# Optimization experiments

Measured on AMD Instinct MI355X. Metric: run time of the kernel, lower is better.

Reference implementation:

```python
import jax, jax.numpy as jnp
import numpy as np

BIT = 128
Y_P = 0.5
RIGHT = BIT / 8.0
LEFT = RIGHT / 2.0
UB = BIT / 2.0
ALPHA = 0.1
PCT_NUM, PCT_DEN = 9, 10  # percent = 9/10
C_COEF = (1.0 / RIGHT) * np.log(Y_P / (99.0 * (1.0 - Y_P)))  # slope c (constant since y_p fixed)
A_COEF = -1.0 / (LEFT * C_COEF) * np.log(99.0 * Y_P / (1.0 - Y_P))  # hard-branch factor a
# with y_p=0.5: d = -c*BP, g = -a*c*BP, so f_easy = c*(x-BP), f_hard = a*c*(x-BP)


def setup_inputs() -> dict:
    key = jax.random.key(0)
    k1, k2 = jax.random.split(key)
    N, C = 6144, 200
    u = jax.random.normal(k1, (N, BIT), dtype=jnp.float32)
    labels = jax.random.randint(k2, (N,), 0, C)
    y = jax.nn.one_hot(labels, C, dtype=jnp.int32)
    ind = jnp.arange(N, dtype=jnp.int32)  # unused dataset indices
    return {"u": u, "y": y, "ind": ind}


def reference(u, y, ind):
    sg = jax.lax.stop_gradient
    N = u.shape[0]
    uh = jnp.tanh(u)
    s = (y @ y.T) > 0                      # [N,N] bool similarity (diagonal is True)
    inner = uh @ uh.T                      # [N,N]
    n_sim = s.sum(axis=1)                  # int per-row similar count
    n_dis = N - n_sim
    fn_sim = n_sim.astype(jnp.float32)
    fn_dis = n_dis.astype(jnp.float32)
    idx = jnp.arange(N)[None, :]

    meanS = jnp.clip(jnp.where(s, inner, 0.0).sum(1) / jnp.maximum(fn_sim, 1.0), 0.0, UB)
    meanDS = jnp.clip(jnp.where(s, 0.0, inner).sum(1) / jnp.maximum(fn_dis, 1.0), 0.0, UB)

    dis_sorted = jnp.sort(jnp.where(s, -jnp.inf, inner), axis=1)
    start_dis = (n_dis * PCT_NUM) // PCT_DEN          # int(len*0.9)
    tail_mask = idx >= (N - n_dis + start_dis)[:, None]
    tail_cnt = jnp.maximum((n_dis - start_dis).astype(jnp.float32), 1.0)
    dMax = jnp.clip(jnp.where(tail_mask, dis_sorted, 0.0).sum(1) / tail_cnt, 0.0, UB)

    sim_sorted = jnp.sort(jnp.where(s, inner, jnp.inf), axis=1)
    start_sim = (n_sim * PCT_NUM) // PCT_DEN
    head_mask = idx < (n_sim - start_sim)[:, None]
    head_cnt = jnp.maximum((n_sim - start_sim).astype(jnp.float32), 1.0)
    sMin = jnp.clip(jnp.where(head_mask, sim_sorted, 0.0).sum(1) / head_cnt, 0.0, UB)

    # .item() in the original detaches these -> stop_gradient
    meanS, meanDS, dMax, sMin = map(sg, (meanS, meanDS, dMax, sMin))
    BP = meanS - (UB - meanS) / UB * jnp.abs(meanS - dMax)      # [N]
    BPd = meanDS + meanDS / UB * jnp.abs(meanDS - sMin)         # [N]

    # similar-pair loss: f + log(1+exp(-f)) == softplus(f)
    dc = inner - BP[:, None]
    f_sim = jnp.where(inner > BP[:, None], C_COEF * dc, A_COEF * C_COEF * dc)
    mask_sim = s & (inner != BP[:, None])             # == BP excluded in torch indexing
    cnt_sim = jnp.maximum(mask_sim.sum(1).astype(jnp.float32), 1.0)
    row_pos = jnp.where(mask_sim, jax.nn.softplus(f_sim), 0.0).sum(1) / cnt_sim

    # dissimilar-pair loss: log(1+exp(-f)) == softplus(-f)
    dcd = inner - BPd[:, None]
    f_dis = jnp.where(inner < BPd[:, None], C_COEF * dcd, A_COEF * C_COEF * dcd)
    mask_dis = (~s) & (inner != BPd[:, None])
    cnt_dis = jnp.maximum(mask_dis.sum(1).astype(jnp.float32), 1.0)
    row_neg = jnp.where(mask_dis, jax.nn.softplus(-f_dis), 0.0).sum(1) / cnt_dis

    valid = (n_sim > 0) & (n_dis > 0)
    count = valid.sum().astype(jnp.float32)
    posL = jnp.where(count > 0, jnp.where(valid, row_pos, 0.0).sum() / jnp.maximum(count, 1.0), 0.0)
    navL = jnp.where(count > 0, jnp.where(valid, row_neg, 0.0).sum() / jnp.maximum(count, 1.0), 0.0)

    q_loss = ALPHA * jnp.mean((uh - jnp.sign(uh)) ** 2)
    return posL + navL + q_loss
```

## Files before the change

### kernel.cpp

```cpp
#include <hip/hip_runtime.h>
#include <cstdint>

#define NROW 6144
#define KDIM 128
#define NLAB 200
#define C_COEF (-0.28719499063341177f)
#define UBV 64.0f

typedef _Float16 f16x8 __attribute__((ext_vector_type(8)));
typedef _Float16 f16x2 __attribute__((ext_vector_type(2)));
typedef float f32x4 __attribute__((ext_vector_type(4)));
typedef __attribute__((address_space(1))) const void as1c_void;
typedef __attribute__((address_space(3))) void as3_void;

union U8 { f16x8 h; unsigned u[4]; f16x2 p[4]; };
union CV16 { _Float16 h; unsigned short us; };

__device__ __forceinline__ float softplus_f(float x){
  return fmaxf(x, 0.f) + __logf(1.f + __expf(-fabsf(x)));
}
__device__ __forceinline__ float waveRedF(float v){
#pragma unroll
  for (int o = 32; o; o >>= 1) v += __shfl_down(v, o, 64);
  return v;
}
__device__ __forceinline__ float bfRedF(float v){
#pragma unroll
  for (int o = 32; o; o >>= 1) v += __shfl_xor(v, o, 64);
  return v;
}
__device__ __forceinline__ int bfRedI(int v){
#pragma unroll
  for (int o = 32; o; o >>= 1) v += __shfl_xor(v, o, 64);
  return v;
}
__device__ __forceinline__ int bfMaxI(int v){
#pragma unroll
  for (int o = 32; o; o >>= 1){ int x = __shfl_xor(v, o, 64); v = v > x ? v : x; }
  return v;
}
__device__ __forceinline__ float bfMaxF(float v){
#pragma unroll
  for (int o = 32; o; o >>= 1) v = fmaxf(v, __shfl_xor(v, o, 64));
  return v;
}
__device__ __forceinline__ float val_of_key(unsigned key){
  unsigned bits = (key & 0x8000u) ? (key ^ 0x8000u) : (key ^ 0xFFFFu);
  CV16 cv; cv.us = (unsigned short)bits;
  return (float)cv.h;
}

__global__ __launch_bounds__(256) void k_labtanh(const int* __restrict__ y,
    unsigned char* __restrict__ lab, int* __restrict__ cnt, int* __restrict__ simIdx,
    const float* __restrict__ u, _Float16* __restrict__ uhswz, float* __restrict__ accf){
  const int bid = blockIdx.x;
  const int tid = threadIdx.x;
  if (bid < NROW){
    if (tid < NLAB && y[(size_t)bid * NLAB + tid] != 0){
      lab[bid] = (unsigned char)tid;
      int p = atomicAdd(&cnt[tid], 1);
      if (p < 512) simIdx[tid * 512 + p] = bid;
    }
    return;
  }
  const int gid = (bid - NROW) * 256 + tid;
  const int row = gid >> 4;
  const int h = gid & 15;
  const int g = h ^ (row & 7);
  const float* sp = u + (size_t)row * KDIM + g * 8;
  float q = 0.f;
  f16x8 o;
#pragma unroll
  for (int t = 0; t < 8; t++){
    float x = sp[t];
    float e2 = __expf(2.f * x);
    float th = 1.f - 2.f * __builtin_amdgcn_rcpf(e2 + 1.f);
    float sg = (th > 0.f) ? 1.f : ((th < 0.f) ? -1.f : 0.f);
    float d = th - sg;
    q += d * d;
    o[t] = (_Float16)th;
  }
  *(f16x8*)(uhswz + (size_t)row * KDIM + h * 8) = o;
  q = waveRedF(q);
  __shared__ float qb[4];
  if ((tid & 63) == 0) qb[tid >> 6] = q;
  __syncthreads();
  if (tid == 0) atomicAdd(&accf[0], qb[0] + qb[1] + qb[2] + qb[3]);
}

__global__ __launch_bounds__(256) void k_mm(const _Float16* __restrict__ A,
    _Float16* __restrict__ out, int row0){
  __shared__ __align__(16) _Float16 SH[2 * 128 * KDIM];
  _Float16* As = SH;
  _Float16* Bs = SH + 128 * KDIM;
  const int tid = threadIdx.x;
  const int wav = tid >> 6, lane = tid & 63;
  const int bj = blockIdx.x, bi = blockIdx.y;

  const char* Ag = (const char*)(A + (size_t)(row0 + bi * 128) * KDIM);
  const char* Bg = (const char*)(A + (size_t)(bj * 128) * KDIM);
  char* Asb = (char*)As;
  char* Bsb = (char*)Bs;
#pragma unroll
  for (int t = 0; t < 8; t++){
    const int ub = wav * 8192 + t * 1024;
    __builtin_amdgcn_global_load_lds((as1c_void*)(Ag + ub + lane * 16),
                                     (as3_void*)(Asb + ub), 16, 0, 0);
    __builtin_amdgcn_global_load_lds((as1c_void*)(Bg + ub + lane * 16),
                                     (as3_void*)(Bsb + ub), 16, 0, 0);
  }
  __syncthreads();

  const int quad = lane >> 4, l16 = lane & 15;
  const int wm = (wav >> 1) * 64, wn = (wav & 1) * 64;
  f32x4 acc[4][4];
#pragma unroll
  for (int im = 0; im < 4; im++)
#pragma unroll
    for (int in = 0; in < 4; in++)
      acc[im][in] = (f32x4){0.f, 0.f, 0.f, 0.f};

#pragma unroll
  for (int kb = 0; kb < 4; kb++){
    f16x8 af[4], bf[4];
#pragma unroll
    for (int i = 0; i < 4; i++){
      const int m = wm + i * 16 + l16;
      const int gidx = kb * 4 + quad;
      af[i] = *(const f16x8*)(Asb + m * 256 + ((gidx ^ (m & 7)) << 4));
      const int n = wn + i * 16 + l16;
      bf[i] = *(const f16x8*)(Bsb + n * 256 + ((gidx ^ (n & 7)) << 4));
    }
#pragma unroll
    for (int im = 0; im < 4; im++)
#pragma unroll
      for (int in = 0; in < 4; in++)
        acc[im][in] = __builtin_amdgcn_mfma_f32_16x16x32_f16(af[im], bf[in], acc[im][in], 0, 0, 0);
  }
  __syncthreads();

  _Float16* Cs = SH;
#pragma unroll
  for (int im = 0; im < 4; im++)
#pragma unroll
    for (int in = 0; in < 4; in++)
#pragma unroll
      for (int r = 0; r < 4; r++){
        const int rl = wm + im * 16 + quad * 4 + r;
        const int cl = wn + in * 16 + l16;
        Cs[rl * 132 + cl] = (_Float16)acc[im][in][r];
      }
  __syncthreads();

  _Float16* obase = out + (size_t)(bi * 128) * NROW + (size_t)bj * 128;
  const int s = tid & 15;
#pragma unroll
  for (int i = 0; i < 8; i++){
    const int r = (tid >> 4) + i * 16;
    f16x8 vv = *(const f16x8*)(Cs + r * 132 + s * 8);
    *(f16x8*)(obase + (size_t)r * NROW + s * 8) = vv;
  }
}

__global__ __launch_bounds__(256) void k_stats(const _Float16* __restrict__ buf,
    const unsigned char* __restrict__ lab, const int* __restrict__ cnt,
    const int* __restrict__ simIdx, float* __restrict__ rowRes, int row0){
  __shared__ int   histS[4][1028];
  __shared__ float simvS[4][512];
  const int tid = threadIdx.x;
  const int lane = tid & 63;
  const int wav = tid >> 6;
  const int lrow = blockIdx.x * 4 + wav;
  const int row = row0 + lrow;
  const int myl = lab[row];
  const int n_sim = cnt[myl];
  const int n_dis = NROW - n_sim;
  if (n_dis == 0 || n_sim == 0) return;
  const int k1 = n_dis - (n_dis * 9) / 10;
  const int k2 = n_sim - (n_sim * 9) / 10;
  const int ns = (n_sim < 512) ? n_sim : 512;

  int*   hist = histS[wav];
  int*   myh  = hist + (lane >> 4) * 257;
  float* simv = simvS[wav];
#pragma unroll
  for (int r = 0; r < 4; r++) *(int4*)&hist[(lane + 64 * r) * 4] = make_int4(0, 0, 0, 0);
  if (lane == 0) *(int4*)&hist[1024] = make_int4(0, 0, 0, 0);

  const f16x8* src = (const f16x8*)(buf + (size_t)lrow * NROW);
  const _Float16* srcs = buf + (size_t)lrow * NROW;

  float sumAll = 0.f;
  const f16x2 ones = (f16x2){(_Float16)1.f, (_Float16)1.f};
#pragma unroll 1
  for (int it = 0; it < 12; ++it){
    U8 x; x.h = src[it * 64 + lane];
#pragma unroll
    for (int k = 0; k < 4; k++){
      unsigned wv = x.u[k];
      unsigned m = (wv >> 15) & 0x00010001u;
      unsigned key2 = wv ^ 0x80008000u ^ (m * 0x7FFFu);
      atomicAdd(&myh[(key2 >> 8) & 0xFFu], 1);
      atomicAdd(&myh[key2 >> 24], 1);
#if __has_builtin(__builtin_amdgcn_fdot2)
      sumAll = __builtin_amdgcn_fdot2(x.p[k], ones, sumAll, false);
#else
      sumAll += (float)x.h[2 * k] + (float)x.h[2 * k + 1];
#endif
    }
  }

  float sumS = 0.f;
  for (int t = lane; t < ns; t += 64){
    int idx = simIdx[myl * 512 + t];
    CV16 cv; cv.h = srcs[idx];
    unsigned bits = (unsigned)cv.us;
    unsigned key = bits ^ 0x8000u ^ ((bits >> 15) * 0x7FFFu);
    float v = (float)cv.h;
    simv[t] = v; sumS += v;
    atomicAdd(&myh[key >> 8], -1);
  }
  sumAll = bfRedF(sumAll);
  sumS = bfRedF(sumS);
  const float sumD = sumAll - sumS;

  int cArr[4];
#pragma unroll
  for (int d = 0; d < 4; d++){
    const int b = 4 * lane + d;
    cArr[d] = hist[b] + hist[257 + b] + hist[514 + b] + hist[771 + b];
  }
  int part = cArr[0] + cArr[1] + cArr[2] + cArr[3];
  int suf = part;
#pragma unroll
  for (int o = 1; o < 64; o <<= 1){
    int x = __shfl_down(suf, o, 64);
    if (lane + o < 64) suf += x;
  }
  int cum = suf - part;
  int encB = -1, krF = 0;
#pragma unroll
  for (int d = 3; d >= 0; --d){
    int cd = cArr[d];
    if (k1 > cum && k1 <= cum + cd){ encB = 4 * lane + d; krF = k1 - cum; }
    cum += cd;
  }
  const int hbStar = bfMaxI(encB);
  const int kr1 = bfMaxI(krF);

#pragma unroll
  for (int r = 0; r < 4; r++) *(int4*)&hist[(lane + 64 * r) * 4] = make_int4(0, 0, 0, 0);
  if (lane == 0) *(int4*)&hist[1024] = make_int4(0, 0, 0, 0);

  float sAb = 0.f;
#pragma unroll 1
  for (int it = 0; it < 12; ++it){
    U8 x; x.h = src[it * 64 + lane];
#pragma unroll
    for (int k = 0; k < 4; k++){
      unsigned wv = x.u[k];
      unsigned m = (wv >> 15) & 0x00010001u;
      unsigned key2 = wv ^ 0x80008000u ^ (m * 0x7FFFu);
      int hbLo = (key2 >> 8) & 0xFF;
      int hbHi = key2 >> 24;
      if (hbLo > hbStar) sAb += (float)x.h[2 * k];
      else if (hbLo == hbStar) atomicAdd(&myh[key2 & 0xFFu], 1);
      if (hbHi > hbStar) sAb += (float)x.h[2 * k + 1];
      else if (hbHi == hbStar) atomicAdd(&myh[(key2 >> 16) & 0xFFu], 1);
    }
  }
  for (int t = lane; t < ns; t += 64){
    float v = simv[t];
    CV16 cv; cv.h = (_Float16)v;
    unsigned bits = (unsigned)cv.us;
    unsigned key = bits ^ 0x8000u ^ ((bits >> 15) * 0x7FFFu);
    int hb = (int)(key >> 8);
    if (hb > hbStar) sAb -= v;
    else if (hb == hbStar) atomicAdd(&myh[key & 0xFFu], -1);
  }
  sAb = bfRedF(sAb);

  int c2[4];
#pragma unroll
  for (int d = 0; d < 4; d++){
    const int b = 4 * lane + d;
    c2[d] = hist[b] + hist[257 + b] + hist[514 + b] + hist[771 + b];
  }
  part = c2[0] + c2[1] + c2[2] + c2[3];
  suf = part;
#pragma unroll
  for (int o = 1; o < 64; o <<= 1){
    int x = __shfl_down(suf, o, 64);
    if (lane + o < 64) suf += x;
  }
  cum = suf - part;
  int encL = -1, g2F = 0;
#pragma unroll
  for (int d = 3; d >= 0; --d){
    int cd = c2[d];
    if (kr1 > cum && kr1 <= cum + cd){ encL = 4 * lane + d; g2F = cum; }
    cum += cd;
  }
  const int lbStar = bfMaxI(encL);
  const int gt2 = bfMaxI(g2F);
  float sumIn = 0.f;
#pragma unroll
  for (int d = 0; d < 4; d++){
    int lb = 4 * lane + d;
    if (lb > lbStar) sumIn += (float)c2[d] * val_of_key((unsigned)((hbStar << 8) | lb));
  }
  sumIn = bfRedF(sumIn);
  const float piv = val_of_key((unsigned)((hbStar << 8) | lbStar));
  const float dSum = sAb + sumIn + (float)(kr1 - gt2) * piv;

  float fpiv2 = -3e38f; int flt = 0;
  for (int t = lane; t < ns; t += 64){
    float vt = simv[t];
    int lt = 0, eq = 0;
    for (int j = 0; j < ns; j++){
      float vj = simv[j];
      lt += (vj < vt); eq += (vj == vt);
    }
    if (lt < k2 && k2 <= lt + eq){ fpiv2 = vt; flt = lt; }
  }
  const float piv2 = bfMaxF(fpiv2);
  const int ltS = bfMaxI(flt);
  float slt = 0.f;
  for (int t = lane; t < ns; t += 64){
    float v = simv[t];
    if (v < piv2) slt += v;
  }
  slt = bfRedF(slt);
  const float sSum = slt + (float)(k2 - ltS) * piv2;

  const float meanS  = fminf(fmaxf(sumS / fmaxf((float)n_sim, 1.f), 0.f), UBV);
  const float meanDS = fminf(fmaxf(sumD / fmaxf((float)n_dis, 1.f), 0.f), UBV);
  const float dMax   = fminf(fmaxf(dSum / fmaxf((float)k1, 1.f), 0.f), UBV);
  const float sMin   = fminf(fmaxf(sSum / fmaxf((float)k2, 1.f), 0.f), UBV);
  const float BP  = meanS - (UBV - meanS) / UBV * fabsf(meanS - dMax);
  const float BPd = meanDS + meanDS / UBV * fabsf(meanDS - sMin);

  float an = 0.f; int ties = 0;
#pragma unroll 1
  for (int it = 0; it < 12; ++it){
    f16x8 h8 = src[it * 64 + lane];
#pragma unroll
    for (int e = 0; e < 8; e++){
      float v = (float)h8[e];
      float dcd = v - BPd;
      float f = ((dcd < 0.f) ? C_COEF : 2.f * C_COEF) * dcd;
      an += softplus_f(-f);
      ties += (dcd == 0.f);
    }
  }
  float spSim = 0.f; int tiesSim = 0;
  float ap = 0.f, cp = 0.f;
  for (int t = lane; t < ns; t += 64){
    float v = simv[t];
    float dcd = v - BPd;
    if (dcd == 0.f) tiesSim++;
    else {
      float f = ((dcd < 0.f) ? C_COEF : 2.f * C_COEF) * dcd;
      spSim += softplus_f(-f);
    }
    if (v != BP){
      float dc = v - BP;
      float f = (v > BP) ? C_COEF * dc : (2.f * C_COEF) * dc;
      ap += softplus_f(f); cp += 1.f;
    }
  }
  an = bfRedF(an); spSim = bfRedF(spSim);
  const int tiesT = bfRedI(ties);
  const int tiesSimT = bfRedI(tiesSim);
  ap = bfRedF(ap); cp = bfRedF(cp);
  if (lane == 0){
    const float L = __logf(1.f + __expf(-0.f));
    float anF = an - (float)tiesT * L - spSim;
    float cnF = (float)(n_dis - (tiesT - tiesSimT));
    float4 r;
    r.x = ap / fmaxf(cp, 1.f);
    r.y = anF / fmaxf(cnF, 1.f);
    r.z = 1.f;
    r.w = 0.f;
    *(float4*)(rowRes + 4 * (size_t)row) = r;
  }
}

__global__ __launch_bounds__(256) void k_final(const float* __restrict__ accf,
    const float* __restrict__ rowRes, float* __restrict__ out){
  const int tid = threadIdx.x;
  float p = 0.f, n = 0.f, c = 0.f;
  for (int i = tid; i < NROW; i += 256){
    float4 r = *(const float4*)(rowRes + 4 * (size_t)i);
    p += r.x; n += r.y; c += r.z;
  }
  p = bfRedF(p); n = bfRedF(n); c = bfRedF(c);
  __shared__ float sb[12];
  const int wav = tid >> 6;
  if ((tid & 63) == 0){ sb[wav] = p; sb[4 + wav] = n; sb[8 + wav] = c; }
  __syncthreads();
  if (tid == 0){
    p = sb[0] + sb[1] + sb[2] + sb[3];
    n = sb[4] + sb[5] + sb[6] + sb[7];
    c = sb[8] + sb[9] + sb[10] + sb[11];
    float posL = 0.f, navL = 0.f;
    if (c > 0.f){ posL = p / c; navL = n / c; }
    out[0] = posL + navL + 0.1f * (accf[0] / (float)(NROW * KDIM));
  }
}

extern "C" void kernel_launch(void* const* d_in, const int* in_sizes, int n_in,
                              void* d_out, int out_size, void* d_ws, size_t ws_size,
                              hipStream_t stream){
  const float* u = (const float*)d_in[0];
  const int* y = (const int*)d_in[1];
  char* ws = (char*)d_ws;
  float* accf = (float*)ws;
  int* cnt = (int*)(ws + 64);
  float* rowRes = (float*)(ws + 4096);
  unsigned char* lab = (unsigned char*)(ws + 102400);
  int* simIdx = (int*)(ws + 108544);
  _Float16* uhswz = (_Float16*)(ws + 518144);
  const size_t ibufOff = 518144 + (size_t)NROW * KDIM * 2;
  _Float16* ibuf = (_Float16*)(ws + ibufOff);

  hipMemsetAsync(d_ws, 0, 102400, stream);
  k_labtanh<<<NROW + (NROW * 16) / 256, 256, 0, stream>>>(y, lab, cnt, simIdx,
                                                          u, uhswz, accf);

  size_t avail = (ws_size > ibufOff) ? ws_size - ibufOff : 0;
  long maxRows = (long)(avail / ((size_t)NROW * 2));
  maxRows = (maxRows / 128) * 128;
  if (maxRows > NROW) maxRows = NROW;
  if (maxRows < 128) maxRows = 128;

  for (int r0 = 0; r0 < NROW; r0 += (int)maxRows){
    int rows = NROW - r0;
    if (rows > maxRows) rows = (int)maxRows;
    k_mm<<<dim3(48, rows / 128), 256, 0, stream>>>(uhswz, ibuf, r0);
    k_stats<<<rows / 4, 256, 0, stream>>>(ibuf, lab, cnt, simIdx, rowRes, r0);
  }
  k_final<<<1, 256, 0, stream>>>(accf, rowRes, (float*)d_out);
}
```

Measured before the change: 170.8 us.

## Process one row per block in stats kernel with row cached in LDS

The stats kernel now assigns a whole 256-thread block to each row instead of one wavefront per row. The row is staged once into shared memory so the second and third passes, and the similar-index gather, read LDS instead of global memory. Reductions now go through cross-wave shared buffers with block barriers, and the second-level histogram is shared by the block. The label kernel is also changed to handle four rows per block using int4 loads. The risk is lower per-block parallelism per row being offset by barrier overhead and higher LDS use per block, which could reduce occupancy.

```diff
diff --git a/kernel.cpp b/kernel.cpp
--- a/kernel.cpp
+++ b/kernel.cpp
@@ -29,19 +29,9 @@
   for (int o = 32; o; o >>= 1) v += __shfl_xor(v, o, 64);
   return v;
 }
-__device__ __forceinline__ int bfRedI(int v){
-#pragma unroll
-  for (int o = 32; o; o >>= 1) v += __shfl_xor(v, o, 64);
-  return v;
-}
 __device__ __forceinline__ int bfMaxI(int v){
 #pragma unroll
   for (int o = 32; o; o >>= 1){ int x = __shfl_xor(v, o, 64); v = v > x ? v : x; }
-  return v;
-}
-__device__ __forceinline__ float bfMaxF(float v){
-#pragma unroll
-  for (int o = 32; o; o >>= 1) v = fmaxf(v, __shfl_xor(v, o, 64));
   return v;
 }
 __device__ __forceinline__ float val_of_key(unsigned key){
@@ -55,15 +45,26 @@
     const float* __restrict__ u, _Float16* __restrict__ uhswz, float* __restrict__ accf){
   const int bid = blockIdx.x;
   const int tid = threadIdx.x;
-  if (bid < NROW){
-    if (tid < NLAB && y[(size_t)bid * NLAB + tid] != 0){
-      lab[bid] = (unsigned char)tid;
-      int p = atomicAdd(&cnt[tid], 1);
-      if (p < 512) simIdx[tid * 512 + p] = bid;
+  const int NLB = NROW / 4;
+  if (bid < NLB){
+    const int lane = tid & 63;
+    const int row = bid * 4 + (tid >> 6);
+    if (lane < NLAB / 4){
+      const int4 v = ((const int4*)(y + (size_t)row * NLAB))[lane];
+      int t = -1;
+      if (v.x != 0) t = 4 * lane;
+      if (v.y != 0) t = 4 * lane + 1;
+      if (v.z != 0) t = 4 * lane + 2;
+      if (v.w != 0) t = 4 * lane + 3;
+      if (t >= 0){
+        lab[row] = (unsigned char)t;
+        int p = atomicAdd(&cnt[t], 1);
+        if (p < 512) simIdx[t * 512 + p] = row;
+      }
     }
     return;
   }
-  const int gid = (bid - NROW) * 256 + tid;
+  const int gid = (bid - NLB) * 256 + tid;
   const int row = gid >> 4;
   const int h = gid & 15;
   const int g = h ^ (row & 7);
@@ -165,12 +166,17 @@
 __global__ __launch_bounds__(256) void k_stats(const _Float16* __restrict__ buf,
     const unsigned char* __restrict__ lab, const int* __restrict__ cnt,
     const int* __restrict__ simIdx, float* __restrict__ rowRes, int row0){
-  __shared__ int   histS[4][1028];
-  __shared__ float simvS[4][512];
+  __shared__ __align__(16) _Float16 rowh[NROW];
+  __shared__ int   hist[4][257];
+  __shared__ int   hist2[257];
+  __shared__ float simv[512];
+  __shared__ float rbuf[32];
+  __shared__ float ctlF[2];
+  __shared__ int   ctlI[2];
   const int tid = threadIdx.x;
   const int lane = tid & 63;
   const int wav = tid >> 6;
-  const int lrow = blockIdx.x * 4 + wav;
+  const int lrow = blockIdx.x;
   const int row = row0 + lrow;
   const int myl = lab[row];
   const int n_sim = cnt[myl];
@@ -180,21 +186,22 @@
   const int k2 = n_sim - (n_sim * 9) / 10;
   const int ns = (n_sim < 512) ? n_sim : 512;
 
-  int*   hist = histS[wav];
-  int*   myh  = hist + (lane >> 4) * 257;
-  float* simv = simvS[wav];
-#pragma unroll
-  for (int r = 0; r < 4; r++) *(int4*)&hist[(lane + 64 * r) * 4] = make_int4(0, 0, 0, 0);
-  if (lane == 0) *(int4*)&hist[1024] = make_int4(0, 0, 0, 0);
+  int* myh = hist[wav];
+#pragma unroll
+  for (int r = 0; r < 4; r++) myh[lane + 64 * r] = 0;
+  if (lane == 0) myh[256] = 0;
+  if (tid < 256) hist2[tid] = 0;
+  if (tid == 0) hist2[256] = 0;
+  __syncthreads();
 
   const f16x8* src = (const f16x8*)(buf + (size_t)lrow * NROW);
-  const _Float16* srcs = buf + (size_t)lrow * NROW;
-
   float sumAll = 0.f;
   const f16x2 ones = (f16x2){(_Float16)1.f, (_Float16)1.f};
-#pragma unroll 1
-  for (int it = 0; it < 12; ++it){
-    U8 x; x.h = src[it * 64 + lane];
+#pragma unroll
+  for (int it = 0; it < 3; ++it){
+    const int g8 = it * 256 + tid;
+    U8 x; x.h = src[g8];
+    ((f16x8*)rowh)[g8] = x.h;
 #pragma unroll
     for (int k = 0; k < 4; k++){
       unsigned wv = x.u[k];
@@ -209,26 +216,38 @@
 #endif
     }
   }
+  sumAll = waveRedF(sumAll);
+  if (lane == 0) rbuf[wav] = sumAll;
+  __syncthreads();
 
   float sumS = 0.f;
-  for (int t = lane; t < ns; t += 64){
+  for (int t = tid; t < ns; t += 256){
     int idx = simIdx[myl * 512 + t];
-    CV16 cv; cv.h = srcs[idx];
+    CV16 cv; cv.h = rowh[idx];
     unsigned bits = (unsigned)cv.us;
     unsigned key = bits ^ 0x8000u ^ ((bits >> 15) * 0x7FFFu);
     float v = (float)cv.h;
     simv[t] = v; sumS += v;
     atomicAdd(&myh[key >> 8], -1);
   }
-  sumAll = bfRedF(sumAll);
-  sumS = bfRedF(sumS);
-  const float sumD = sumAll - sumS;
+  sumS = waveRedF(sumS);
+  if (lane == 0) rbuf[4 + wav] = sumS;
+  __syncthreads();
+
+  const float sumAllT = rbuf[0] + rbuf[1] + rbuf[2] + rbuf[3];
+  const float sumST   = rbuf[4] + rbuf[5] + rbuf[6] + rbuf[7];
+  const float sumD = sumAllT - sumST;
 
   int cArr[4];
-#pragma unroll
-  for (int d = 0; d < 4; d++){
-    const int b = 4 * lane + d;
-    cArr[d] = hist[b] + hist[257 + b] + hist[514 + b] + hist[771 + b];
+  {
+    int4 a = *(const int4*)&hist[0][4 * lane];
+    int4 b = *(const int4*)&hist[1][4 * lane];
+    int4 c = *(const int4*)&hist[2][4 * lane];
+    int4 d = *(const int4*)&hist[3][4 * lane];
+    cArr[0] = a.x + b.x + c.x + d.x;
+    cArr[1] = a.y + b.y + c.y + d.y;
+    cArr[2] = a.z + b.z + c.z + d.z;
+    cArr[3] = a.w + b.w + c.w + d.w;
   }
   int part = cArr[0] + cArr[1] + cArr[2] + cArr[3];
   int suf = part;
@@ -248,14 +267,10 @@
   const int hbStar = bfMaxI(encB);
   const int kr1 = bfMaxI(krF);
 
-#pragma unroll
-  for (int r = 0; r < 4; r++) *(int4*)&hist[(lane + 64 * r) * 4] = make_int4(0, 0, 0, 0);
-  if (lane == 0) *(int4*)&hist[1024] = make_int4(0, 0, 0, 0);
-
   float sAb = 0.f;
-#pragma unroll 1
-  for (int it = 0; it < 12; ++it){
-    U8 x; x.h = src[it * 64 + lane];
+#pragma unroll
+  for (int it = 0; it < 3; ++it){
+    U8 x; x.h = ((const f16x8*)rowh)[it * 256 + tid];
 #pragma unroll
     for (int k = 0; k < 4; k++){
       unsigned wv = x.u[k];
@@ -264,28 +279,28 @@
       int hbLo = (key2 >> 8) & 0xFF;
       int hbHi = key2 >> 24;
       if (hbLo > hbStar) sAb += (float)x.h[2 * k];
-      else if (hbLo == hbStar) atomicAdd(&myh[key2 & 0xFFu], 1);
+      else if (hbLo == hbStar) atomicAdd(&hist2[key2 & 0xFFu], 1);
       if (hbHi > hbStar) sAb += (float)x.h[2 * k + 1];
-      else if (hbHi == hbStar) atomicAdd(&myh[(key2 >> 16) & 0xFFu], 1);
-    }
-  }
-  for (int t = lane; t < ns; t += 64){
+      else if (hbHi == hbStar) atomicAdd(&hist2[(key2 >> 16) & 0xFFu], 1);
+    }
+  }
+  for (int t = tid; t < ns; t += 256){
     float v = simv[t];
     CV16 cv; cv.h = (_Float16)v;
     unsigned bits = (unsigned)cv.us;
     unsigned key = bits ^ 0x8000u ^ ((bits >> 15) * 0x7FFFu);
     int hb = (int)(key >> 8);
     if (hb > hbStar) sAb -= v;
-    else if (hb == hbStar) atomicAdd(&myh[key & 0xFFu], -1);
-  }
-  sAb = bfRedF(sAb);
+    else if (hb == hbStar) atomicAdd(&hist2[key & 0xFFu], -1);
+  }
+  sAb = waveRedF(sAb);
+  if (lane == 0) rbuf[8 + wav] = sAb;
+  __syncthreads();
+  const float sAbT = rbuf[8] + rbuf[9] + rbuf[10] + rbuf[11];
 
   int c2[4];
-#pragma unroll
-  for (int d = 0; d < 4; d++){
-    const int b = 4 * lane + d;
-    c2[d] = hist[b] + hist[257 + b] + hist[514 + b] + hist[771 + b];
-  }
+  { int4 c4 = *(const int4*)&hist2[4 * lane];
+    c2[0] = c4.x; c2[1] = c4.y; c2[2] = c4.z; c2[3] = c4.w; }
   part = c2[0] + c2[1] + c2[2] + c2[3];
   suf = part;
 #pragma unroll
@@ -311,29 +326,32 @@
   }
   sumIn = bfRedF(sumIn);
   const float piv = val_of_key((unsigned)((hbStar << 8) | lbStar));
-  const float dSum = sAb + sumIn + (float)(kr1 - gt2) * piv;
-
-  float fpiv2 = -3e38f; int flt = 0;
-  for (int t = lane; t < ns; t += 64){
+  const float dSum = sAbT + sumIn + (float)(kr1 - gt2) * piv;
+
+  for (int t = tid; t < ns; t += 256){
     float vt = simv[t];
     int lt = 0, eq = 0;
     for (int j = 0; j < ns; j++){
       float vj = simv[j];
       lt += (vj < vt); eq += (vj == vt);
     }
-    if (lt < k2 && k2 <= lt + eq){ fpiv2 = vt; flt = lt; }
-  }
-  const float piv2 = bfMaxF(fpiv2);
-  const int ltS = bfMaxI(flt);
+    if (lt < k2 && k2 <= lt + eq){ ctlF[0] = vt; ctlI[0] = lt; }
+  }
+  __syncthreads();
+  const float piv2 = ctlF[0];
+  const int ltS = ctlI[0];
   float slt = 0.f;
-  for (int t = lane; t < ns; t += 64){
+  for (int t = tid; t < ns; t += 256){
     float v = simv[t];
     if (v < piv2) slt += v;
   }
-  slt = bfRedF(slt);
-  const float sSum = slt + (float)(k2 - ltS) * piv2;
-
-  const float meanS  = fminf(fmaxf(sumS / fmaxf((float)n_sim, 1.f), 0.f), UBV);
+  slt = waveRedF(slt);
+  if (lane == 0) rbuf[12 + wav] = slt;
+  __syncthreads();
+  const float sltT = rbuf[12] + rbuf[13] + rbuf[14] + rbuf[15];
+  const float sSum = sltT + (float)(k2 - ltS) * piv2;
+
+  const float meanS  = fminf(fmaxf(sumST / fmaxf((float)n_sim, 1.f), 0.f), UBV);
   const float meanDS = fminf(fmaxf(sumD / fmaxf((float)n_dis, 1.f), 0.f), UBV);
   const float dMax   = fminf(fmaxf(dSum / fmaxf((float)k1, 1.f), 0.f), UBV);
   const float sMin   = fminf(fmaxf(sSum / fmaxf((float)k2, 1.f), 0.f), UBV);
@@ -341,9 +359,9 @@
   const float BPd = meanDS + meanDS / UBV * fabsf(meanDS - sMin);
 
   float an = 0.f; int ties = 0;
-#pragma unroll 1
-  for (int it = 0; it < 12; ++it){
-    f16x8 h8 = src[it * 64 + lane];
+#pragma unroll
+  for (int it = 0; it < 3; ++it){
+    f16x8 h8 = ((const f16x8*)rowh)[it * 256 + tid];
 #pragma unroll
     for (int e = 0; e < 8; e++){
       float v = (float)h8[e];
@@ -355,7 +373,7 @@
   }
   float spSim = 0.f; int tiesSim = 0;
   float ap = 0.f, cp = 0.f;
-  for (int t = lane; t < ns; t += 64){
+  for (int t = tid; t < ns; t += 256){
     float v = simv[t];
     float dcd = v - BPd;
     if (dcd == 0.f) tiesSim++;
@@ -369,16 +387,27 @@
       ap += softplus_f(f); cp += 1.f;
     }
   }
-  an = bfRedF(an); spSim = bfRedF(spSim);
-  const int tiesT = bfRedI(ties);
-  const int tiesSimT = bfRedI(tiesSim);
-  ap = bfRedF(ap); cp = bfRedF(cp);
+  an = waveRedF(an); ap = waveRedF(ap); cp = waveRedF(cp);
+  spSim = waveRedF(spSim);
+  float tiesF = waveRedF((float)ties);
+  float tiesSimF = waveRedF((float)tiesSim);
   if (lane == 0){
+    rbuf[wav] = an; rbuf[4 + wav] = ap; rbuf[8 + wav] = cp;
+    rbuf[16 + wav] = spSim; rbuf[20 + wav] = tiesF; rbuf[24 + wav] = tiesSimF;
+  }
+  __syncthreads();
+  if (tid == 0){
+    float anT = rbuf[0] + rbuf[1] + rbuf[2] + rbuf[3];
+    float apT = rbuf[4] + rbuf[5] + rbuf[6] + rbuf[7];
+    float cpT = rbuf[8] + rbuf[9] + rbuf[10] + rbuf[11];
+    float spT = rbuf[16] + rbuf[17] + rbuf[18] + rbuf[19];
+    float tiesT = rbuf[20] + rbuf[21] + rbuf[22] + rbuf[23];
+    float tiesSimT = rbuf[24] + rbuf[25] + rbuf[26] + rbuf[27];
     const float L = __logf(1.f + __expf(-0.f));
-    float anF = an - (float)tiesT * L - spSim;
-    float cnF = (float)(n_dis - (tiesT - tiesSimT));
+    float anF = anT - tiesT * L - spT;
+    float cnF = (float)n_dis - (tiesT - tiesSimT);
     float4 r;
-    r.x = ap / fmaxf(cp, 1.f);
+    r.x = apT / fmaxf(cpT, 1.f);
     r.y = anF / fmaxf(cnF, 1.f);
     r.z = 1.f;
     r.w = 0.f;
@@ -425,8 +454,8 @@
   _Float16* ibuf = (_Float16*)(ws + ibufOff);
 
   hipMemsetAsync(d_ws, 0, 102400, stream);
-  k_labtanh<<<NROW + (NROW * 16) / 256, 256, 0, stream>>>(y, lab, cnt, simIdx,
-                                                          u, uhswz, accf);
+  k_labtanh<<<NROW / 4 + (NROW * 16) / 256, 256, 0, stream>>>(y, lab, cnt, simIdx,
+                                                              u, uhswz, accf);
 
   size_t avail = (ws_size > ibufOff) ? ws_size - ibufOff : 0;
   long maxRows = (long)(avail / ((size_t)NROW * 2));
@@ -438,7 +467,7 @@
     int rows = NROW - r0;
     if (rows > maxRows) rows = (int)maxRows;
     k_mm<<<dim3(48, rows / 128), 256, 0, stream>>>(uhswz, ibuf, r0);
-    k_stats<<<rows / 4, 256, 0, stream>>>(ibuf, lab, cnt, simIdx, rowRes, r0);
+    k_stats<<<rows, 256, 0, stream>>>(ibuf, lab, cnt, simIdx, rowRes, r0);
   }
   k_final<<<1, 256, 0, stream>>>(accf, rowRes, (float*)d_out);
 }
```

Measured after the change: 178.0 us. +4.2%, slower.
